# Kernel optimization log

Hardware: AMD Instinct MI355X
Metric: run time of the kernel (lower is better)

## Reference

```python
import jax, jax.numpy as jnp
import numpy as np

N = 100000   # nodes
E = 1600000  # edges
G = 512      # graphs in batch
F_IN = 128
H = 128
F_OUT = 1


def setup_inputs() -> dict:
    key = jax.random.key(0)
    ks = jax.random.split(key, 12)
    x = jax.random.normal(ks[0], (N, F_IN), dtype=jnp.float32)
    src = jax.random.randint(ks[1], (E,), 0, N, dtype=jnp.int32)
    dst = jax.random.randint(ks[2], (E,), 0, N, dtype=jnp.int32)
    node2graph = jnp.sort(jax.random.randint(ks[3], (N,), 0, G, dtype=jnp.int32))
    s_in = 1.0 / np.sqrt(F_IN)
    s_h = 1.0 / np.sqrt(H)
    W0 = jax.random.normal(ks[4], (F_IN, H), dtype=jnp.float32) * s_in
    b0 = jnp.zeros((H,), dtype=jnp.float32)
    W1 = jax.random.normal(ks[5], (H, H), dtype=jnp.float32) * s_h
    b1 = jnp.zeros((H,), dtype=jnp.float32)
    W2 = jax.random.normal(ks[6], (H, H), dtype=jnp.float32) * s_h
    b2 = jnp.zeros((H,), dtype=jnp.float32)
    Wm1 = jax.random.normal(ks[7], (H, H), dtype=jnp.float32) * s_h
    bm1 = jnp.zeros((H,), dtype=jnp.float32)
    Wm2 = jax.random.normal(ks[8], (H, F_OUT), dtype=jnp.float32) * s_h
    bm2 = jnp.zeros((F_OUT,), dtype=jnp.float32)
    return {"x": x, "src": src, "dst": dst, "node2graph": node2graph,
            "W0": W0, "b0": b0, "W1": W1, "b1": b1, "W2": W2, "b2": b2,
            "Wm1": Wm1, "bm1": bm1, "Wm2": Wm2, "bm2": bm2}


def _degree_norms(src, dst):
    ones = jnp.ones((E,), dtype=jnp.float32)
    out_deg = jax.ops.segment_sum(ones, src, num_segments=N)
    in_deg = jax.ops.segment_sum(ones, dst, num_segments=N)
    norm_out = jax.lax.rsqrt(jnp.maximum(out_deg, 1.0))  # [N]
    norm_in = jax.lax.rsqrt(jnp.maximum(in_deg, 1.0))    # [N]
    return norm_out, norm_in


def _graph_conv(x, src, dst, norm_out, norm_in, W, b):
    # DGL GraphConv, norm='both', in_feats <= out_feats path:
    # aggregate normalized src features, then linear + activation.
    xs = x * norm_out[:, None]
    msg = xs[src]                                         # [E, H] gather
    agg = jax.ops.segment_sum(msg, dst, num_segments=N)   # [N, H] scatter-add
    agg = agg * norm_in[:, None]
    return jax.nn.relu(agg @ W + b)


def reference(x, src, dst, node2graph, W0, b0, W1, b1, W2, b2, Wm1, bm1, Wm2, bm2):
    norm_out, norm_in = _degree_norms(src, dst)
    h = _graph_conv(x, src, dst, norm_out, norm_in, W0, b0)
    h = _graph_conv(h, src, dst, norm_out, norm_in, W1, b1)
    h = _graph_conv(h, src, dst, norm_out, norm_in, W2, b2)
    # sum_nodes readout per graph
    g = jax.ops.segment_sum(h, node2graph, num_segments=G)  # [G, H]
    # MLP head: Linear -> ReLU -> Linear
    return jax.nn.relu(g @ Wm1 + bm1) @ Wm2 + bm2           # [G, 1]
```

## Files before the change

### kernel.cpp

```cpp
#include <hip/hip_runtime.h>

#define NN 100000
#define NE 1600000
#define NG 512
#define HD 128

#define NBK 196
#define CHUNK 5120
#define NC 313
#define LH (2 * NBK * NC)

typedef _Float16 half4 __attribute__((ext_vector_type(4)));
typedef _Float16 h8 __attribute__((ext_vector_type(8)));
typedef float f32x4 __attribute__((ext_vector_type(4)));

__global__ __launch_bounds__(256) void k_hist(const int* __restrict__ src,
                                              const int* __restrict__ dst,
                                              int* __restrict__ H) {
    __shared__ int hd[NBK], hs[NBK];
    int c = blockIdx.x;
    for (int i = threadIdx.x; i < NBK; i += 256) { hd[i] = 0; hs[i] = 0; }
    __syncthreads();
    int e0 = c * CHUNK;
    int e1 = e0 + CHUNK; if (e1 > NE) e1 = NE;
    for (int e = e0 + threadIdx.x; e < e1; e += 256) {
        atomicAdd(&hd[dst[e] >> 9], 1);
        atomicAdd(&hs[src[e] >> 9], 1);
    }
    __syncthreads();
    for (int i = threadIdx.x; i < NBK; i += 256) {
        H[i * NC + c] = hd[i];
        H[NBK * NC + i * NC + c] = hs[i];
    }
}

__global__ __launch_bounds__(256) void k_scan1g(int* __restrict__ H,
                                                int* __restrict__ bsum, int L) {
    __shared__ int s[256];
    int i = blockIdx.x * 256 + threadIdx.x;
    int v = (i < L) ? H[i] : 0;
    s[threadIdx.x] = v;
    __syncthreads();
    for (int off = 1; off < 256; off <<= 1) {
        int t = (threadIdx.x >= off) ? s[threadIdx.x - off] : 0;
        __syncthreads();
        s[threadIdx.x] += t;
        __syncthreads();
    }
    if (i < L) H[i] = s[threadIdx.x] - v;
    if (threadIdx.x == 255) bsum[blockIdx.x] = s[255];
}

__global__ __launch_bounds__(512) void k_scan2(int* __restrict__ bsum, int nb) {
    __shared__ int s[512];
    int v = (threadIdx.x < nb) ? bsum[threadIdx.x] : 0;
    s[threadIdx.x] = v;
    __syncthreads();
    for (int off = 1; off < 512; off <<= 1) {
        int t = (threadIdx.x >= off) ? s[threadIdx.x - off] : 0;
        __syncthreads();
        s[threadIdx.x] += t;
        __syncthreads();
    }
    if (threadIdx.x < nb) bsum[threadIdx.x] = s[threadIdx.x] - v;
}

__global__ __launch_bounds__(256) void k_scan3g(int* __restrict__ H,
                                                const int* __restrict__ bsum, int L) {
    int i = blockIdx.x * 256 + threadIdx.x;
    if (i < L) H[i] += bsum[i >> 8];
}

__global__ __launch_bounds__(256) void k_scatter(const int* __restrict__ src,
                                                 const int* __restrict__ dst,
                                                 const int* __restrict__ H,
                                                 int2* __restrict__ dpart,
                                                 int* __restrict__ spart) {
    __shared__ int cd[NBK], cs[NBK];
    int c = blockIdx.x;
    for (int i = threadIdx.x; i < NBK; i += 256) {
        cd[i] = H[i * NC + c];
        cs[i] = H[NBK * NC + i * NC + c] - NE;
    }
    __syncthreads();
    int e0 = c * CHUNK;
    int e1 = e0 + CHUNK; if (e1 > NE) e1 = NE;
    for (int e = e0 + threadIdx.x; e < e1; e += 256) {
        int s = src[e], d = dst[e];
        int pd = atomicAdd(&cd[d >> 9], 1);
        dpart[pd] = make_int2(s, d);
        int ps = atomicAdd(&cs[s >> 9], 1);
        spart[ps] = s;
    }
}

__global__ __launch_bounds__(256) void k_bucket(const int2* __restrict__ dpart,
                                                const int* __restrict__ spart,
                                                const int* __restrict__ H,
                                                int* __restrict__ offs,
                                                int* __restrict__ csr,
                                                float* __restrict__ ni,
                                                float* __restrict__ no) {
    __shared__ int deg[512];
    __shared__ int cur[512];
    __shared__ int tmp[256];
    int b = blockIdx.x;
    bool isDst = (b < NBK);
    int bb = isDst ? b : b - NBK;
    int start, end;
    if (isDst) {
        start = H[bb * NC];
        end = (bb + 1 < NBK) ? H[(bb + 1) * NC] : NE;
    } else {
        start = H[NBK * NC + bb * NC] - NE;
        end = (bb + 1 < NBK) ? H[NBK * NC + (bb + 1) * NC] - NE : NE;
    }
    for (int i = threadIdx.x; i < 512; i += 256) deg[i] = 0;
    __syncthreads();
    if (isDst) {
        for (int i = start + threadIdx.x; i < end; i += 256)
            atomicAdd(&deg[dpart[i].y & 511], 1);
    } else {
        for (int i = start + threadIdx.x; i < end; i += 256)
            atomicAdd(&deg[spart[i] & 511], 1);
    }
    __syncthreads();
    int vb = bb * 512;
    if (!isDst) {
        for (int i = threadIdx.x; i < 512; i += 256) {
            int v = vb + i;
            if (v < NN) no[v] = rsqrtf(fmaxf((float)deg[i], 1.0f));
        }
        return;
    }
    int t = threadIdx.x;
    int a0 = deg[2 * t], a1 = deg[2 * t + 1];
    int pair = a0 + a1;
    tmp[t] = pair;
    __syncthreads();
    for (int off = 1; off < 256; off <<= 1) {
        int v2 = (t >= off) ? tmp[t - off] : 0;
        __syncthreads();
        tmp[t] += v2;
        __syncthreads();
    }
    int ex = tmp[t] - pair;
    cur[2 * t] = start + ex;
    cur[2 * t + 1] = start + ex + a0;
    __syncthreads();
    for (int i = threadIdx.x; i < 512; i += 256) {
        int v = vb + i;
        if (v < NN) {
            offs[v] = cur[i];
            ni[v] = rsqrtf(fmaxf((float)deg[i], 1.0f));
        }
    }
    if (b == NBK - 1 && threadIdx.x == 0) offs[NN] = NE;
    __syncthreads();
    for (int i = start + threadIdx.x; i < end; i += 256) {
        int2 e = dpart[i];
        int p = atomicAdd(&cur[e.y & 511], 1);
        csr[p] = e.x;
    }
}

__global__ __launch_bounds__(256) void k_castw(const float* __restrict__ W0,
                                               const float* __restrict__ W1,
                                               const float* __restrict__ W2,
                                               _Float16* __restrict__ Bt) {
    int i = blockIdx.x * 256 + threadIdx.x;
    if (i >= 3 * 16384) return;
    int w = i >> 14;
    int rem = i & 16383;
    int n = rem >> 7;
    int k = rem & 127;
    const float* W = (w == 0) ? W0 : ((w == 1) ? W1 : W2);
    Bt[i] = (_Float16)W[k * 128 + n];
}

template <typename TA>
__global__ __launch_bounds__(256) void k_gemm_mfma(const TA* __restrict__ A,
                                                   const _Float16* __restrict__ Bt,
                                                   const float* __restrict__ no,
                                                   _Float16* __restrict__ Zh,
                                                   int nrows) {
    __shared__ _Float16 Bs[128 * 136];
    int tid = threadIdx.x;
    {
        const h8* B8 = (const h8*)Bt;
        h8* Bs8 = (h8*)Bs;
        for (int i = tid; i < 2048; i += 256) {
            int n = i >> 4, c = i & 15;
            Bs8[n * 17 + c] = B8[i];
        }
    }

    int wave = tid >> 6;
    int lane = tid & 63;
    int m16 = lane & 15;
    int quad = lane >> 4;
    int rowbase = blockIdx.x * 64 + wave * 16;
    int row = rowbase + m16;
    bool valid = row < nrows;

    h8 afrag[4];
    if (valid) {
        if constexpr (sizeof(TA) == 2) {
            const h8* Arow = (const h8*)(A + (size_t)row * 128);
#pragma unroll
            for (int kk = 0; kk < 4; kk++) afrag[kk] = Arow[kk * 4 + quad];
        } else {
            const float4* Arow = (const float4*)(A + (size_t)row * 128);
#pragma unroll
            for (int kk = 0; kk < 4; kk++) {
                float4 lo = Arow[kk * 8 + quad * 2];
                float4 hi = Arow[kk * 8 + quad * 2 + 1];
                h8 a;
                a[0] = (_Float16)lo.x; a[1] = (_Float16)lo.y;
                a[2] = (_Float16)lo.z; a[3] = (_Float16)lo.w;
                a[4] = (_Float16)hi.x; a[5] = (_Float16)hi.y;
                a[6] = (_Float16)hi.z; a[7] = (_Float16)hi.w;
                afrag[kk] = a;
            }
        }
    } else {
#pragma unroll
        for (int kk = 0; kk < 4; kk++) {
            h8 a;
#pragma unroll
            for (int j = 0; j < 8; j++) a[j] = (_Float16)0.f;
            afrag[kk] = a;
        }
    }

    __syncthreads();

    f32x4 acc[8];
#pragma unroll
    for (int nt = 0; nt < 8; nt++) acc[nt] = (f32x4){0.f, 0.f, 0.f, 0.f};

    const h8* Bs8 = (const h8*)Bs;
#pragma unroll
    for (int nt = 0; nt < 8; nt++) {
        const h8* Bp = Bs8 + (size_t)(nt * 16 + m16) * 17;
#pragma unroll
        for (int kk = 0; kk < 4; kk++) {
            acc[nt] = __builtin_amdgcn_mfma_f32_16x16x32_f16(afrag[kk], Bp[kk * 4 + quad],
                                                             acc[nt], 0, 0, 0);
        }
    }

    float nor[4];
#pragma unroll
    for (int r = 0; r < 4; r++) {
        int grow = rowbase + quad * 4 + r;
        nor[r] = (grow < nrows) ? no[grow] : 0.f;
    }
#pragma unroll
    for (int nt = 0; nt < 8; nt++) {
#pragma unroll
        for (int r = 0; r < 4; r++) {
            int grow = rowbase + quad * 4 + r;
            if (grow < nrows)
                Zh[(size_t)grow * 128 + nt * 16 + m16] = (_Float16)(acc[nt][r] * nor[r]);
        }
    }
}

__global__ __launch_bounds__(128) void k_agg(const h8* __restrict__ Zh,
                                             const int* __restrict__ offs,
                                             const int* __restrict__ csr,
                                             const float* __restrict__ ni,
                                             const float* __restrict__ b,
                                             h8* __restrict__ H16) {
    int v = blockIdx.x * 8 + (threadIdx.x >> 4);
    int c = threadIdx.x & 15;
    int s = offs[v];
    int e = offs[v + 1];
    float a0[8], a1[8];
#pragma unroll
    for (int j = 0; j < 8; j++) { a0[j] = 0.f; a1[j] = 0.f; }
    int i = s;
    for (; i + 4 <= e; i += 4) {
        int u0 = csr[i];
        int u1 = csr[i + 1];
        int u2 = csr[i + 2];
        int u3 = csr[i + 3];
        h8 z0 = Zh[(size_t)u0 * 16 + c];
        h8 z1 = Zh[(size_t)u1 * 16 + c];
        h8 z2 = Zh[(size_t)u2 * 16 + c];
        h8 z3 = Zh[(size_t)u3 * 16 + c];
#pragma unroll
        for (int j = 0; j < 8; j++) {
            a0[j] += (float)z0[j] + (float)z1[j];
            a1[j] += (float)z2[j] + (float)z3[j];
        }
    }
    for (; i < e; i++) {
        int u = csr[i];
        h8 z = Zh[(size_t)u * 16 + c];
#pragma unroll
        for (int j = 0; j < 8; j++) a0[j] += (float)z[j];
    }
    float niv = ni[v];
    const float* bb = b + c * 8;
    h8 r;
#pragma unroll
    for (int j = 0; j < 8; j++)
        r[j] = (_Float16)fmaxf((a0[j] + a1[j]) * niv + bb[j], 0.f);
    H16[(size_t)v * 16 + c] = r;
}

__global__ __launch_bounds__(128) void k_readout(const _Float16* __restrict__ H,
                                                 const int* __restrict__ n2g,
                                                 float* __restrict__ g) {
    int f = threadIdx.x;
    int v0 = blockIdx.x * 128;
    int vend = v0 + 128;
    if (vend > NN) vend = NN;
    float acc = 0.f;
    int cur = n2g[v0];
    for (int v = v0; v < vend; v++) {
        int gid = n2g[v];
        if (gid != cur) {
            atomicAdd(&g[cur * 128 + f], acc);
            acc = 0.f;
            cur = gid;
        }
        acc += (float)H[(size_t)v * 128 + f];
    }
    atomicAdd(&g[cur * 128 + f], acc);
}

__global__ __launch_bounds__(128) void k_head(const float* __restrict__ g,
                                              const float* __restrict__ Wm1,
                                              const float* __restrict__ bm1,
                                              const float* __restrict__ Wm2,
                                              const float* __restrict__ bm2,
                                              float* __restrict__ out) {
    __shared__ float gs[128];
    __shared__ float red[128];
    int gi = blockIdx.x;
    int f = threadIdx.x;
    gs[f] = g[gi * 128 + f];
    __syncthreads();
    float acc = bm1[f];
    for (int k = 0; k < 128; k++) acc += gs[k] * Wm1[k * 128 + f];
    float h1 = fmaxf(acc, 0.f);
    red[f] = h1 * Wm2[f];
    __syncthreads();
    for (int s2 = 64; s2 > 0; s2 >>= 1) {
        if (f < s2) red[f] += red[f + s2];
        __syncthreads();
    }
    if (f == 0) out[gi] = red[0] + bm2[0];
}

extern "C" void kernel_launch(void* const* d_in, const int* in_sizes, int n_in,
                              void* d_out, int out_size, void* d_ws, size_t ws_size,
                              hipStream_t stream) {
    const float* x   = (const float*)d_in[0];
    const int*   src = (const int*)d_in[1];
    const int*   dst = (const int*)d_in[2];
    const int*   n2g = (const int*)d_in[3];
    const float* W0  = (const float*)d_in[4];
    const float* b0  = (const float*)d_in[5];
    const float* W1  = (const float*)d_in[6];
    const float* b1  = (const float*)d_in[7];
    const float* W2  = (const float*)d_in[8];
    const float* b2  = (const float*)d_in[9];
    const float* Wm1 = (const float*)d_in[10];
    const float* bm1 = (const float*)d_in[11];
    const float* Wm2 = (const float*)d_in[12];
    const float* bm2 = (const float*)d_in[13];
    float* out = (float*)d_out;

    char* p = (char*)d_ws;
    auto carve = [&](size_t bytes) -> char* {
        char* r = p;
        p += (bytes + 255) & ~(size_t)255;
        return r;
    };
    _Float16* zh  = (_Float16*)carve((size_t)NN * HD * 2);
    _Float16* h16 = (_Float16*)carve((size_t)NN * HD * 2);
    _Float16* Bt  = (_Float16*)carve((size_t)3 * 128 * 128 * 2);
    float* no     = (float*)carve((size_t)NN * 4);
    float* ni     = (float*)carve((size_t)NN * 4);
    int*   offs   = (int*)carve((size_t)(NN + 1) * 4);
    int*   csr    = (int*)carve((size_t)NE * 4);
    int*   Hh     = (int*)carve((size_t)LH * 4);
    int*   bsum   = (int*)carve((size_t)512 * 4);
    int2*  dpart  = (int2*)carve((size_t)NE * 8);
    int*   spart  = (int*)carve((size_t)NE * 4);
    float* g      = (float*)carve((size_t)NG * HD * 4);

    hipMemsetAsync(g, 0, (size_t)NG * HD * 4, stream);

    k_castw<<<(3 * 16384 + 255) / 256, 256, 0, stream>>>(W0, W1, W2, Bt);

    int scan_blocks = (LH + 255) / 256;
    k_hist<<<NC, 256, 0, stream>>>(src, dst, Hh);
    k_scan1g<<<scan_blocks, 256, 0, stream>>>(Hh, bsum, LH);
    k_scan2<<<1, 512, 0, stream>>>(bsum, scan_blocks);
    k_scan3g<<<scan_blocks, 256, 0, stream>>>(Hh, bsum, LH);
    k_scatter<<<NC, 256, 0, stream>>>(src, dst, Hh, dpart, spart);
    k_bucket<<<2 * NBK, 256, 0, stream>>>(dpart, spart, Hh, offs, csr, ni, no);

    int gemm_blocks = (NN + 63) / 64;

    k_gemm_mfma<float><<<gemm_blocks, 256, 0, stream>>>(x, Bt, no, zh, NN);
    k_agg<<<NN / 8, 128, 0, stream>>>((const h8*)zh, offs, csr, ni, b0, (h8*)h16);
    k_gemm_mfma<_Float16><<<gemm_blocks, 256, 0, stream>>>(h16, Bt + 16384, no, zh, NN);
    k_agg<<<NN / 8, 128, 0, stream>>>((const h8*)zh, offs, csr, ni, b1, (h8*)h16);
    k_gemm_mfma<_Float16><<<gemm_blocks, 256, 0, stream>>>(h16, Bt + 32768, no, zh, NN);
    k_agg<<<NN / 8, 128, 0, stream>>>((const h8*)zh, offs, csr, ni, b2, (h8*)h16);

    k_readout<<<(NN + 127) / 128, 128, 0, stream>>>(h16, n2g, g);
    k_head<<<NG, 128, 0, stream>>>(g, Wm1, bm1, Wm2, bm2, out);
}
```

Measured before the change: 457.7 us.

## Split aggregation feature dimension into two halves for cache-resident gathers

The GEMM now writes its output as two separate 64-column fp16 arrays, and each aggregation layer runs as two passes, one per half. Each half is 12.8 MB, so the random neighbor gathers have a smaller working set that may fit better in L2/MALL cache. The cost is reading the CSR index arrays twice per layer and paying extra kernel launches, and each gathered row fetch is now only 128 bytes.

```diff
diff --git a/kernel.cpp b/kernel.cpp
--- a/kernel.cpp
+++ b/kernel.cpp
@@ -182,7 +182,8 @@
 __global__ __launch_bounds__(256) void k_gemm_mfma(const TA* __restrict__ A,
                                                    const _Float16* __restrict__ Bt,
                                                    const float* __restrict__ no,
-                                                   _Float16* __restrict__ Zh,
+                                                   _Float16* __restrict__ Zlo,
+                                                   _Float16* __restrict__ Zhi,
                                                    int nrows) {
     __shared__ _Float16 Bs[128 * 136];
     int tid = threadIdx.x;
@@ -258,23 +259,26 @@
     }
 #pragma unroll
     for (int nt = 0; nt < 8; nt++) {
+        _Float16* Zp = (nt < 4) ? Zlo : Zhi;
+        int col = (nt & 3) * 16 + m16;
 #pragma unroll
         for (int r = 0; r < 4; r++) {
             int grow = rowbase + quad * 4 + r;
             if (grow < nrows)
-                Zh[(size_t)grow * 128 + nt * 16 + m16] = (_Float16)(acc[nt][r] * nor[r]);
-        }
-    }
-}
-
-__global__ __launch_bounds__(128) void k_agg(const h8* __restrict__ Zh,
+                Zp[(size_t)grow * 64 + col] = (_Float16)(acc[nt][r] * nor[r]);
+        }
+    }
+}
+
+__global__ __launch_bounds__(128) void k_agg(const h8* __restrict__ Zp,
                                              const int* __restrict__ offs,
                                              const int* __restrict__ csr,
                                              const float* __restrict__ ni,
                                              const float* __restrict__ b,
-                                             h8* __restrict__ H16) {
-    int v = blockIdx.x * 8 + (threadIdx.x >> 4);
-    int c = threadIdx.x & 15;
+                                             h8* __restrict__ H16,
+                                             int phase) {
+    int v = blockIdx.x * 16 + (threadIdx.x >> 3);
+    int c = threadIdx.x & 7;
     int s = offs[v];
     int e = offs[v + 1];
     float a0[8], a1[8];
@@ -286,10 +290,10 @@
         int u1 = csr[i + 1];
         int u2 = csr[i + 2];
         int u3 = csr[i + 3];
-        h8 z0 = Zh[(size_t)u0 * 16 + c];
-        h8 z1 = Zh[(size_t)u1 * 16 + c];
-        h8 z2 = Zh[(size_t)u2 * 16 + c];
-        h8 z3 = Zh[(size_t)u3 * 16 + c];
+        h8 z0 = Zp[(size_t)u0 * 8 + c];
+        h8 z1 = Zp[(size_t)u1 * 8 + c];
+        h8 z2 = Zp[(size_t)u2 * 8 + c];
+        h8 z3 = Zp[(size_t)u3 * 8 + c];
 #pragma unroll
         for (int j = 0; j < 8; j++) {
             a0[j] += (float)z0[j] + (float)z1[j];
@@ -298,17 +302,17 @@
     }
     for (; i < e; i++) {
         int u = csr[i];
-        h8 z = Zh[(size_t)u * 16 + c];
+        h8 z = Zp[(size_t)u * 8 + c];
 #pragma unroll
         for (int j = 0; j < 8; j++) a0[j] += (float)z[j];
     }
     float niv = ni[v];
-    const float* bb = b + c * 8;
+    const float* bb = b + phase * 64 + c * 8;
     h8 r;
 #pragma unroll
     for (int j = 0; j < 8; j++)
         r[j] = (_Float16)fmaxf((a0[j] + a1[j]) * niv + bb[j], 0.f);
-    H16[(size_t)v * 16 + c] = r;
+    H16[(size_t)v * 16 + phase * 8 + c] = r;
 }
 
 __global__ __launch_bounds__(128) void k_readout(const _Float16* __restrict__ H,
@@ -381,7 +385,8 @@
         p += (bytes + 255) & ~(size_t)255;
         return r;
     };
-    _Float16* zh  = (_Float16*)carve((size_t)NN * HD * 2);
+    _Float16* zL  = (_Float16*)carve((size_t)NN * 64 * 2);
+    _Float16* zH  = (_Float16*)carve((size_t)NN * 64 * 2);
     _Float16* h16 = (_Float16*)carve((size_t)NN * HD * 2);
     _Float16* Bt  = (_Float16*)carve((size_t)3 * 128 * 128 * 2);
     float* no     = (float*)carve((size_t)NN * 4);
@@ -407,13 +412,17 @@
     k_bucket<<<2 * NBK, 256, 0, stream>>>(dpart, spart, Hh, offs, csr, ni, no);
 
     int gemm_blocks = (NN + 63) / 64;
-
-    k_gemm_mfma<float><<<gemm_blocks, 256, 0, stream>>>(x, Bt, no, zh, NN);
-    k_agg<<<NN / 8, 128, 0, stream>>>((const h8*)zh, offs, csr, ni, b0, (h8*)h16);
-    k_gemm_mfma<_Float16><<<gemm_blocks, 256, 0, stream>>>(h16, Bt + 16384, no, zh, NN);
-    k_agg<<<NN / 8, 128, 0, stream>>>((const h8*)zh, offs, csr, ni, b1, (h8*)h16);
-    k_gemm_mfma<_Float16><<<gemm_blocks, 256, 0, stream>>>(h16, Bt + 32768, no, zh, NN);
-    k_agg<<<NN / 8, 128, 0, stream>>>((const h8*)zh, offs, csr, ni, b2, (h8*)h16);
+    int agg_blocks  = NN / 16;
+
+    k_gemm_mfma<float><<<gemm_blocks, 256, 0, stream>>>(x, Bt, no, zL, zH, NN);
+    k_agg<<<agg_blocks, 128, 0, stream>>>((const h8*)zL, offs, csr, ni, b0, (h8*)h16, 0);
+    k_agg<<<agg_blocks, 128, 0, stream>>>((const h8*)zH, offs, csr, ni, b0, (h8*)h16, 1);
+    k_gemm_mfma<_Float16><<<gemm_blocks, 256, 0, stream>>>(h16, Bt + 16384, no, zL, zH, NN);
+    k_agg<<<agg_blocks, 128, 0, stream>>>((const h8*)zL, offs, csr, ni, b1, (h8*)h16, 0);
+    k_agg<<<agg_blocks, 128, 0, stream>>>((const h8*)zH, offs, csr, ni, b1, (h8*)h16, 1);
+    k_gemm_mfma<_Float16><<<gemm_blocks, 256, 0, stream>>>(h16, Bt + 32768, no, zL, zH, NN);
+    k_agg<<<agg_blocks, 128, 0, stream>>>((const h8*)zL, offs, csr, ni, b2, (h8*)h16, 0);
+    k_agg<<<agg_blocks, 128, 0, stream>>>((const h8*)zH, offs, csr, ni, b2, (h8*)h16, 1);
 
     k_readout<<<(NN + 127) / 128, 128, 0, stream>>>(h16, n2g, g);
     k_head<<<NG, 128, 0, stream>>>(g, Wm1, bm1, Wm2, bm2, out);
```

Result: no change. 462.7 us (+1.1%).

## Restructure readout to one block per graph with binary-searched node ranges

Applied to the files above, without the earlier changes.

The readout kernel now launches one block per graph. Each block binary-searches the sorted node-to-graph array to find its node range, accumulates with 16-byte half8 vector loads across 8 row slots, and reduces in shared memory before writing the result directly. This removes the global atomics and the memset of the graph buffer. Load balance now depends on graph sizes, and each block pays for two small binary searches.

```diff
diff --git a/kernel.cpp b/kernel.cpp
--- a/kernel.cpp
+++ b/kernel.cpp
@@ -311,25 +311,46 @@
     H16[(size_t)v * 16 + c] = r;
 }
 
-__global__ __launch_bounds__(128) void k_readout(const _Float16* __restrict__ H,
+__global__ __launch_bounds__(128) void k_readout(const h8* __restrict__ H8,
                                                  const int* __restrict__ n2g,
                                                  float* __restrict__ g) {
-    int f = threadIdx.x;
-    int v0 = blockIdx.x * 128;
-    int vend = v0 + 128;
-    if (vend > NN) vend = NN;
-    float acc = 0.f;
-    int cur = n2g[v0];
-    for (int v = v0; v < vend; v++) {
-        int gid = n2g[v];
-        if (gid != cur) {
-            atomicAdd(&g[cur * 128 + f], acc);
-            acc = 0.f;
-            cur = gid;
-        }
-        acc += (float)H[(size_t)v * 128 + f];
-    }
-    atomicAdd(&g[cur * 128 + f], acc);
+    __shared__ float red[128 * 8];
+    int gi = blockIdx.x;
+    int t = threadIdx.x;
+    int slot = t >> 4;
+    int c = t & 15;
+
+    int lo = 0, hi = NN;
+    while (lo < hi) { int mid = (lo + hi) >> 1; if (n2g[mid] < gi) lo = mid + 1; else hi = mid; }
+    int s = lo;
+    hi = NN;
+    while (lo < hi) { int mid = (lo + hi) >> 1; if (n2g[mid] < gi + 1) lo = mid + 1; else hi = mid; }
+    int e = lo;
+
+    float acc[8];
+#pragma unroll
+    for (int j = 0; j < 8; j++) acc[j] = 0.f;
+    for (int v = s + slot; v < e; v += 8) {
+        h8 z = H8[(size_t)v * 16 + c];
+#pragma unroll
+        for (int j = 0; j < 8; j++) acc[j] += (float)z[j];
+    }
+#pragma unroll
+    for (int j = 0; j < 8; j++) red[t * 8 + j] = acc[j];
+    __syncthreads();
+    for (int off = 4; off >= 1; off >>= 1) {
+        if (slot < off) {
+#pragma unroll
+            for (int j = 0; j < 8; j++)
+                red[t * 8 + j] += red[(t + off * 16) * 8 + j];
+        }
+        __syncthreads();
+    }
+    if (slot == 0) {
+#pragma unroll
+        for (int j = 0; j < 8; j++)
+            g[gi * 128 + c * 8 + j] = red[t * 8 + j];
+    }
 }
 
 __global__ __launch_bounds__(128) void k_head(const float* __restrict__ g,
@@ -394,8 +415,6 @@
     int*   spart  = (int*)carve((size_t)NE * 4);
     float* g      = (float*)carve((size_t)NG * HD * 4);
 
-    hipMemsetAsync(g, 0, (size_t)NG * HD * 4, stream);
-
     k_castw<<<(3 * 16384 + 255) / 256, 256, 0, stream>>>(W0, W1, W2, Bt);
 
     int scan_blocks = (LH + 255) / 256;
@@ -415,6 +434,6 @@
     k_gemm_mfma<_Float16><<<gemm_blocks, 256, 0, stream>>>(h16, Bt + 32768, no, zh, NN);
     k_agg<<<NN / 8, 128, 0, stream>>>((const h8*)zh, offs, csr, ni, b2, (h8*)h16);
 
-    k_readout<<<(NN + 127) / 128, 128, 0, stream>>>(h16, n2g, g);
+    k_readout<<<NG, 128, 0, stream>>>((const h8*)h16, n2g, g);
     k_head<<<NG, 128, 0, stream>>>(g, Wm1, bm1, Wm2, bm2, out);
 }
```

Measured after the change: 438.4 us. -4.2%, faster.
